# Kernel tuning notes

Measured on AMD Instinct MI355X. Metric: run time of the kernel, lower is better.

The kernel has to match this reference:

```python
import jax, jax.numpy as jnp
import numpy as np

N_HEAD = 16

def setup_inputs() -> dict:
    key = jax.random.key(0)
    ks = jax.random.split(key, 4)
    C = 2048
    x = jax.random.normal(ks[0], (4, 2048, C), dtype=jnp.float32)
    # weights stored [in, out] (transpose of torch Linear's [out, in]); same math y = x @ W + b
    w_qkv = jax.random.normal(ks[1], (C, 3 * C), dtype=jnp.float32) * (1.0 / np.sqrt(C))
    b_qkv = jnp.zeros((3 * C,), dtype=jnp.float32)
    w_proj = jax.random.normal(ks[2], (C, C), dtype=jnp.float32) * (1.0 / np.sqrt(C))
    b_proj = jnp.zeros((C,), dtype=jnp.float32)
    return {"x": x, "w_qkv": w_qkv, "b_qkv": b_qkv, "w_proj": w_proj, "b_proj": b_proj}

def reference(x, w_qkv, b_qkv, w_proj, b_proj):
    B, S, C = x.shape
    H = N_HEAD
    D = C // H
    qkv = x @ w_qkv + b_qkv                      # [B,S,3C]
    q, k, v = jnp.split(qkv, 3, axis=-1)
    # [B,H,S,D]
    q = q.reshape(B, S, H, D).transpose(0, 2, 1, 3)
    k = k.reshape(B, S, H, D).transpose(0, 2, 1, 3)
    v = v.reshape(B, S, H, D).transpose(0, 2, 1, 3)
    scale = 1.0 / np.sqrt(D).astype(np.float32)
    scores = jnp.einsum('bhqd,bhkd->bhqk', q, k) * scale   # [B,H,S,S]
    causal = jnp.tril(jnp.ones((S, S), dtype=bool))
    scores = jnp.where(causal, scores, jnp.finfo(scores.dtype).min)
    attn = jax.nn.softmax(scores, axis=-1)
    y = jnp.einsum('bhqk,bhkd->bhqd', attn, v)              # [B,H,S,D]
    y = y.transpose(0, 2, 1, 3).reshape(B, S, C)
    return y @ w_proj + b_proj
```

## Files before the change

### kernel.cpp

```cpp
#include <hip/hip_runtime.h>
#include <hip/hip_bf16.h>

typedef __bf16 bf16x8 __attribute__((ext_vector_type(8)));
typedef float floatx4 __attribute__((ext_vector_type(4)));

__device__ __forceinline__ unsigned short f2bf(float f) {
  unsigned u = __float_as_uint(f);
  u += 0x7fffu + ((u >> 16) & 1u);
  return (unsigned short)(u >> 16);
}

__device__ __forceinline__ unsigned cvt_pk_bf16(float lo, float hi) {
  unsigned r;
  asm("v_cvt_pk_bf16_f32 %0, %1, %2" : "=v"(r) : "v"(lo), "v"(hi));
  return r;
}

__device__ __forceinline__ void async_copy16(const void* g, void* l) {
  __builtin_amdgcn_global_load_lds(
      (const __attribute__((address_space(1))) void*)g,
      (__attribute__((address_space(3))) void*)l, 16, 0, 0);
}

__global__ __launch_bounds__(256) void cvt_bf16(
    const float* __restrict__ in, unsigned short* __restrict__ out) {
  size_t i = ((size_t)blockIdx.x * 256 + threadIdx.x) * 8;
  float4 a0 = *(const float4*)&in[i];
  float4 a1 = *(const float4*)&in[i + 4];
  uint4 d;
  d.x = (unsigned)f2bf(a0.x) | ((unsigned)f2bf(a0.y) << 16);
  d.y = (unsigned)f2bf(a0.z) | ((unsigned)f2bf(a0.w) << 16);
  d.z = (unsigned)f2bf(a1.x) | ((unsigned)f2bf(a1.y) << 16);
  d.w = (unsigned)f2bf(a1.z) | ((unsigned)f2bf(a1.w) << 16);
  *(uint4*)(&out[i]) = d;
}

__global__ __launch_bounds__(256) void transpose_cvt(
    const float* __restrict__ in, unsigned short* __restrict__ out,
    int R, int Ccol) {
  __shared__ unsigned short tile[32][33];
  int c0 = blockIdx.x * 32, r0 = blockIdx.y * 32;
  int tx = threadIdx.x & 31, ty = threadIdx.x >> 5;
  #pragma unroll
  for (int i = 0; i < 32; i += 8)
    tile[ty + i][tx] = f2bf(in[(size_t)(r0 + ty + i) * Ccol + c0 + tx]);
  __syncthreads();
  #pragma unroll
  for (int i = 0; i < 32; i += 8)
    out[(size_t)(c0 + ty + i) * R + r0 + tx] = tile[tx][ty + i];
}

__device__ __forceinline__ void stage_tile256(
    const unsigned short* __restrict__ A, const unsigned short* __restrict__ Bt,
    int K, int m0, int n0, int k0,
    unsigned short* As, unsigned short* Bs, int lane, int w) {
  const int lrow = lane >> 3;
  const int gch = (lane & 7) ^ lrow;
  #pragma unroll
  for (int u = 0; u < 4; u++) {
    int g = w * 4 + u;
    int row = g * 8 + lrow;
    async_copy16(&A[(size_t)(m0 + row) * K + k0 + gch * 8], &As[g * 512]);
  }
  #pragma unroll
  for (int u = 0; u < 4; u++) {
    int g = w * 4 + u;
    int row = g * 8 + lrow;
    async_copy16(&Bt[(size_t)(n0 + row) * K + k0 + gch * 8], &Bs[g * 512]);
  }
}

__device__ __forceinline__ void gemm_bt_256(
    const unsigned short* __restrict__ A, const unsigned short* __restrict__ Bt,
    int K, int m0, int n0,
    unsigned short* AsB, unsigned short* BsB,
    floatx4 acc[8][4]) {
  const int t = threadIdx.x, lane = t & 63, w = t >> 6;
  const int wr = w >> 2, wc = w & 3;
  const int l15 = lane & 15, l4 = lane >> 4;
  const floatx4 zf = {0.f, 0.f, 0.f, 0.f};
  #pragma unroll
  for (int mi = 0; mi < 8; mi++)
    #pragma unroll
    for (int ni = 0; ni < 4; ni++) acc[mi][ni] = zf;

  const int nkt = K >> 6;
  stage_tile256(A, Bt, K, m0, n0, 0, AsB, BsB, lane, w);
  __syncthreads();

  #pragma unroll 1
  for (int kt = 0; kt < nkt; kt++) {
    const unsigned short* Ab = AsB + (kt & 1) * 16384;
    const unsigned short* Bb = BsB + (kt & 1) * 16384;
    if (kt + 1 < nkt)
      stage_tile256(A, Bt, K, m0, n0, (kt + 1) * 64,
                    AsB + ((kt + 1) & 1) * 16384,
                    BsB + ((kt + 1) & 1) * 16384, lane, w);
    #pragma unroll
    for (int j = 0; j < 4; j++) {
      const int qm = j >> 1, qn = j & 1;
      bf16x8 af[4][2], bfr[2][2];
      #pragma unroll
      for (int mi = 0; mi < 4; mi++) {
        int row = wr * 128 + (qm * 4 + mi) * 16 + l15;
        #pragma unroll
        for (int kk = 0; kk < 2; kk++)
          af[mi][kk] = *(const bf16x8*)(
              &Ab[row * 64 + (((kk * 4 + l4) ^ (l15 & 7)) << 3)]);
      }
      #pragma unroll
      for (int ni = 0; ni < 2; ni++) {
        int row = wc * 64 + (qn * 2 + ni) * 16 + l15;
        #pragma unroll
        for (int kk = 0; kk < 2; kk++)
          bfr[ni][kk] = *(const bf16x8*)(
              &Bb[row * 64 + (((kk * 4 + l4) ^ (l15 & 7)) << 3)]);
      }
      __builtin_amdgcn_s_barrier();
      __builtin_amdgcn_s_setprio(1);
      #pragma unroll
      for (int kk = 0; kk < 2; kk++)
        #pragma unroll
        for (int mi = 0; mi < 4; mi++)
          #pragma unroll
          for (int ni = 0; ni < 2; ni++)
            acc[qm * 4 + mi][qn * 2 + ni] = __builtin_amdgcn_mfma_f32_16x16x32_bf16(
                af[mi][kk], bfr[ni][kk], acc[qm * 4 + mi][qn * 2 + ni], 0, 0, 0);
      __builtin_amdgcn_s_setprio(0);
      if (j < 3) __builtin_amdgcn_s_barrier();
    }
    __syncthreads();
  }
}

__global__ __launch_bounds__(512, 2) void gemm_qkv(
    const unsigned short* __restrict__ X, const unsigned short* __restrict__ WT,
    const float* __restrict__ bias,
    unsigned short* __restrict__ Qo, unsigned short* __restrict__ Ko,
    unsigned short* __restrict__ Vto) {
  __shared__ unsigned short As[2][256 * 64];
  __shared__ unsigned short Bs[2][256 * 64];
  int id = blockIdx.x;
  int n8 = gridDim.x >> 3;
  int lg = (id & 7) * n8 + (id >> 3);
  int bm = lg & 31, bn = lg >> 5;
  int m0 = bm * 256, n0 = bn * 256;
  floatx4 acc[8][4];
  gemm_bt_256(X, WT, 2048, m0, n0, As[0], Bs[0], acc);

  const int t = threadIdx.x, lane = t & 63, w = t >> 6;
  const int wr = w >> 2, wc = w & 3;
  const int l15 = lane & 15, l4 = lane >> 4;
  int which = n0 >> 11;
  int b = m0 >> 11;
  int s0 = m0 & 2047;
  float bv[4];
  #pragma unroll
  for (int ni = 0; ni < 4; ni++)
    bv[ni] = bias[n0 + wc * 64 + ni * 16 + l15];

  if (which < 2) {
    unsigned short* dst = (which == 0) ? Qo : Ko;
    #pragma unroll
    for (int ni = 0; ni < 4; ni++) {
      int cn = (n0 & 2047) + wc * 64 + ni * 16;
      int h = cn >> 7, d = (cn & 127) + l15;
      size_t base = ((size_t)(b * 16 + h)) * 2048;
      #pragma unroll
      for (int mi = 0; mi < 8; mi++) {
        #pragma unroll
        for (int r = 0; r < 4; r++) {
          int srow = s0 + wr * 128 + mi * 16 + l4 * 4 + r;
          dst[(base + srow) * 128 + d] = f2bf(acc[mi][ni][r] + bv[ni]);
        }
      }
    }
  } else {
    #pragma unroll
    for (int ni = 0; ni < 4; ni++) {
      int cn = (n0 & 2047) + wc * 64 + ni * 16;
      int h = cn >> 7, d = (cn & 127) + l15;
      #pragma unroll
      for (int mi = 0; mi < 8; mi++) {
        int sr = s0 + wr * 128 + mi * 16 + l4 * 4;
        ushort4 v;
        v.x = f2bf(acc[mi][ni][0] + bv[ni]);
        v.y = f2bf(acc[mi][ni][1] + bv[ni]);
        v.z = f2bf(acc[mi][ni][2] + bv[ni]);
        v.w = f2bf(acc[mi][ni][3] + bv[ni]);
        *(ushort4*)(&Vto[((size_t)(b * 16 + h) * 128 + d) * 2048 + sr]) = v;
      }
    }
  }
}

__device__ __forceinline__ void attn_stage(
    const unsigned short* __restrict__ Kb, const unsigned short* __restrict__ Vb,
    __bf16* Ksel, __bf16* Vsel, int k0, int lane, int w) {
  const int krow_in = lane >> 4, kch = lane & 15;
  const int vrow_in = lane >> 3, vch = lane & 7;
  #pragma unroll
  for (int u = 0; u < 2; u++) {
    int uk = w * 2 + u;
    int row = uk * 4 + krow_in;
    int sch = kch ^ (row & 7);
    async_copy16(&Kb[(size_t)(k0 + row) * 128 + sch * 8], Ksel + uk * 512);
  }
  #pragma unroll
  for (int u = 0; u < 2; u++) {
    int uv = w * 2 + u;
    int row = uv * 8 + vrow_in;
    int sch = vch ^ vrow_in;
    async_copy16(&Vb[(size_t)row * 2048 + k0 + sch * 8], Vsel + uv * 512);
  }
}

__global__ __launch_bounds__(512, 4) void attn(
    const unsigned short* __restrict__ Qg, const unsigned short* __restrict__ Kg,
    const unsigned short* __restrict__ Vtg, unsigned short* __restrict__ Yg) {
  const int S = 2048, Dh = 128;
  const float c1 = 0.08838834764831845f * 1.4426950408889634f;
  const float NEG_BIG = -3.0e38f;
  __shared__ __bf16 Ks[2][64 * 128];
  __shared__ __bf16 Vs[2][128 * 64];
  __shared__ __bf16 Ps[8][16 * 64];

  int wg = blockIdx.x;
  int lg = (wg & 7) * 64 + (wg >> 3);
  int qtp = lg & 7;
  int bh = lg >> 3;
  const int t = threadIdx.x, lane = t & 63, w = t >> 6;
  const int l15 = lane & 15, l4 = lane >> 4;
  const unsigned short* Qb = Qg + (size_t)bh * S * Dh;
  const unsigned short* Kb = Kg + (size_t)bh * S * Dh;
  const unsigned short* Vb = Vtg + (size_t)bh * Dh * S;
  __bf16* Pw = Ps[w];
  int b = bh >> 4, h = bh & 15;
  const floatx4 zf = {0.f, 0.f, 0.f, 0.f};

  #pragma unroll 1
  for (int half = 0; half < 2; half++) {
    int jq = half ? qtp : (15 - qtp);
    int qb0 = jq * 128;
    int qrow_base = qb0 + w * 16;
    bf16x8 qf[4];
    #pragma unroll
    for (int kk = 0; kk < 4; kk++)
      qf[kk] = *(const bf16x8*)(
          &Qb[(size_t)(qrow_base + l15) * Dh + kk * 32 + l4 * 8]);
    floatx4 accO[8];
    #pragma unroll
    for (int nd = 0; nd < 8; nd++) accO[nd] = zf;
    float mst = NEG_BIG, lst = 0.f;

    int ntiles = 2 * jq + 2;
    int cur = 0;
    attn_stage(Kb, Vb, Ks[0], Vs[0], 0, lane, w);
    __syncthreads();

    #pragma unroll 1
    for (int kt = 0; kt < ntiles; kt++) {
      if (kt + 1 < ntiles)
        attn_stage(Kb, Vb, Ks[cur ^ 1], Vs[cur ^ 1], (kt + 1) * 64, lane, w);

      const __bf16* Kcur = Ks[cur];
      const __bf16* Vcur = Vs[cur];
      floatx4 sc[4];
      #pragma unroll
      for (int ni = 0; ni < 4; ni++) sc[ni] = zf;
      __builtin_amdgcn_s_setprio(1);
      #pragma unroll
      for (int kk = 0; kk < 4; kk++) {
        bf16x8 kf[4];
        #pragma unroll
        for (int ni = 0; ni < 4; ni++) {
          int row = ni * 16 + l15;
          kf[ni] = *(const bf16x8*)(
              &Kcur[row * 128 + (((kk * 4 + l4) ^ (l15 & 7)) << 3)]);
        }
        #pragma unroll
        for (int ni = 0; ni < 4; ni++)
          sc[ni] = __builtin_amdgcn_mfma_f32_16x16x32_bf16(kf[ni], qf[kk], sc[ni], 0, 0, 0);
      }
      __builtin_amdgcn_s_setprio(0);

      if (kt >= 2 * jq) {
        int kb = kt * 64 - qb0 - w * 16 - l15;
        #pragma unroll
        for (int ni = 0; ni < 4; ni++)
          #pragma unroll
          for (int r = 0; r < 4; r++)
            if (kb + ni * 16 + l4 * 4 + r > 0) sc[ni][r] = NEG_BIG;
      }

      float mt = fmaxf(fmaxf(fmaxf(sc[0][0], sc[0][1]), fmaxf(sc[0][2], sc[0][3])),
                       fmaxf(fmaxf(sc[1][0], sc[1][1]), fmaxf(sc[1][2], sc[1][3])));
      mt = fmaxf(mt,
           fmaxf(fmaxf(fmaxf(sc[2][0], sc[2][1]), fmaxf(sc[2][2], sc[2][3])),
                 fmaxf(fmaxf(sc[3][0], sc[3][1]), fmaxf(sc[3][2], sc[3][3]))));
      mt = fmaxf(mt, __shfl_xor(mt, 16, 64));
      mt = fmaxf(mt, __shfl_xor(mt, 32, 64));

      if (!__all(mt <= mst + 8.0f)) {
        float mnew = fmaxf(mst, mt);
        float alpha = exp2f((mst - mnew) * c1);
        mst = mnew;
        lst *= alpha;
        float ar[4];
        #pragma unroll
        for (int r = 0; r < 4; r++)
          ar[r] = __shfl(alpha, l4 * 20 + r, 64);
        #pragma unroll
        for (int nd = 0; nd < 8; nd++)
          #pragma unroll
          for (int r = 0; r < 4; r++) accO[nd][r] *= ar[r];
      }

      float mc = mst * c1;
      float p[4][4];
      float rs = 0.f;
      #pragma unroll
      for (int ni = 0; ni < 4; ni++)
        #pragma unroll
        for (int r = 0; r < 4; r++) {
          p[ni][r] = exp2f(sc[ni][r] * c1 - mc);
          rs += p[ni][r];
        }
      rs += __shfl_xor(rs, 16, 64);
      rs += __shfl_xor(rs, 32, 64);
      lst += rs;

      #pragma unroll
      for (int ni = 0; ni < 4; ni++) {
        uint2 dw;
        dw.x = cvt_pk_bf16(p[ni][0], p[ni][1]);
        dw.y = cvt_pk_bf16(p[ni][2], p[ni][3]);
        int s = ni * 4 + l4;
        *(uint2*)(&Pw[l15 * 64 + (((s >> 1) ^ (l15 & 7)) << 3) + ((s & 1) << 2)]) = dw;
      }

      __builtin_amdgcn_s_setprio(1);
      #pragma unroll
      for (int kk = 0; kk < 2; kk++) {
        bf16x8 pf = *(const bf16x8*)(
            &Pw[l15 * 64 + (((kk * 4 + l4) ^ (l15 & 7)) << 3)]);
        #pragma unroll
        for (int nd = 0; nd < 8; nd++) {
          int row = nd * 16 + l15;
          bf16x8 vf = *(const bf16x8*)(
              &Vcur[row * 64 + (((kk * 4 + l4) ^ (l15 & 7)) << 3)]);
          accO[nd] = __builtin_amdgcn_mfma_f32_16x16x32_bf16(pf, vf, accO[nd], 0, 0, 0);
        }
      }
      __builtin_amdgcn_s_setprio(0);
      __syncthreads();
      cur ^= 1;
    }

    float invl = 1.0f / lst;
    float ivr[4];
    #pragma unroll
    for (int r = 0; r < 4; r++)
      ivr[r] = __shfl(invl, l4 * 20 + r, 64);
    #pragma unroll
    for (int r = 0; r < 4; r++) {
      int srow = qrow_base + l4 * 4 + r;
      size_t rowbase = ((size_t)(b * 2048 + srow)) * 2048 + h * 128;
      #pragma unroll
      for (int nd = 0; nd < 8; nd++)
        Yg[rowbase + nd * 16 + l15] = f2bf(accO[nd][r] * ivr[r]);
    }
  }
}

__global__ __launch_bounds__(512, 2) void gemm_proj(
    const unsigned short* __restrict__ Yin, const unsigned short* __restrict__ WT,
    const float* __restrict__ bias, float* __restrict__ Og) {
  __shared__ unsigned short As[2][256 * 64];
  __shared__ unsigned short Bs[2][256 * 64];
  int id = blockIdx.x;
  int n8 = gridDim.x >> 3;
  int lg = (id & 7) * n8 + (id >> 3);
  int bm = lg & 31, bn = lg >> 5;
  int m0 = bm * 256, n0 = bn * 256;
  floatx4 acc[8][4];
  gemm_bt_256(Yin, WT, 2048, m0, n0, As[0], Bs[0], acc);

  const int t = threadIdx.x, lane = t & 63, w = t >> 6;
  const int wr = w >> 2, wc = w & 3;
  const int l15 = lane & 15, l4 = lane >> 4;
  float bv[4];
  #pragma unroll
  for (int ni = 0; ni < 4; ni++)
    bv[ni] = bias[n0 + wc * 64 + ni * 16 + l15];
  #pragma unroll
  for (int mi = 0; mi < 8; mi++)
    #pragma unroll
    for (int ni = 0; ni < 4; ni++)
      #pragma unroll
      for (int r = 0; r < 4; r++)
        Og[(size_t)(m0 + wr * 128 + mi * 16 + l4 * 4 + r) * 2048 +
           n0 + wc * 64 + ni * 16 + l15] = acc[mi][ni][r] + bv[ni];
}

extern "C" void kernel_launch(void* const* d_in, const int* in_sizes, int n_in,
                              void* d_out, int out_size, void* d_ws, size_t ws_size,
                              hipStream_t stream) {
  const float* x      = (const float*)d_in[0];
  const float* w_qkv  = (const float*)d_in[1];
  const float* b_qkv  = (const float*)d_in[2];
  const float* w_proj = (const float*)d_in[3];
  const float* b_proj = (const float*)d_in[4];
  float* out = (float*)d_out;
  char* ws = (char*)d_ws;

  unsigned short* Q   = (unsigned short*)d_out;
  unsigned short* Kt  = (unsigned short*)((char*)d_out + 33554432);
  unsigned short* Vt  = (unsigned short*)(ws);
  unsigned short* Xbf = (unsigned short*)(ws + 33554432);
  unsigned short* Y   = (unsigned short*)(ws + 33554432);
  unsigned short* WqT = (unsigned short*)(ws + 67108864);
  unsigned short* WpT = (unsigned short*)(ws + 67108864);

  cvt_bf16<<<dim3(8192), 256, 0, stream>>>(x, Xbf);
  transpose_cvt<<<dim3(192, 64), 256, 0, stream>>>(w_qkv, WqT, 2048, 6144);
  gemm_qkv<<<dim3(768), 512, 0, stream>>>(Xbf, WqT, b_qkv, Q, Kt, Vt);
  attn<<<dim3(512), 512, 0, stream>>>(Q, Kt, Vt, Y);
  transpose_cvt<<<dim3(64, 64), 256, 0, stream>>>(w_proj, WpT, 2048, 2048);
  gemm_proj<<<dim3(256), 512, 0, stream>>>(Y, WpT, b_proj, out);
}
```

Measured before the change: 681.6 us.

## Interleave next-tile async loads across MFMA sub-phases and change block-to-tile mapping

The GEMM mainloop now issues the prefetch of the next K-tile in four chunks, one per compute sub-phase, instead of all at once at the start of the iteration. It uses explicit vmcnt waits plus s_barrier in place of the per-iteration __syncthreads, so the wait only covers the current tile's loads. Both GEMMs also drop the XCD-aware block swizzle for a plain row-major grid mapping (bn fastest), which changes L2 locality across chiplets. The finer-grained pipeline spreads memory traffic between MFMA bursts, but the vmcnt accounting and barrier placement must stay exactly right to avoid LDS races.

Measured after the change: 590.0 us. 1.16x faster.

```diff
diff --git a/kernel.cpp b/kernel.cpp
--- a/kernel.cpp
+++ b/kernel.cpp
@@ -50,23 +50,26 @@
     out[(size_t)(c0 + ty + i) * R + r0 + tx] = tile[tx][ty + i];
 }
 
-__device__ __forceinline__ void stage_tile256(
+__device__ __forceinline__ void stage_chunk256(
     const unsigned short* __restrict__ A, const unsigned short* __restrict__ Bt,
     int K, int m0, int n0, int k0,
-    unsigned short* As, unsigned short* Bs, int lane, int w) {
+    unsigned short* As, unsigned short* Bs, int lane, int w, int j) {
   const int lrow = lane >> 3;
   const int gch = (lane & 7) ^ lrow;
-  #pragma unroll
-  for (int u = 0; u < 4; u++) {
-    int g = w * 4 + u;
-    int row = g * 8 + lrow;
-    async_copy16(&A[(size_t)(m0 + row) * K + k0 + gch * 8], &As[g * 512]);
-  }
-  #pragma unroll
-  for (int u = 0; u < 4; u++) {
-    int g = w * 4 + u;
-    int row = g * 8 + lrow;
-    async_copy16(&Bt[(size_t)(n0 + row) * K + k0 + gch * 8], &Bs[g * 512]);
+  if (j < 2) {
+    #pragma unroll
+    for (int u = 2 * j; u < 2 * j + 2; u++) {
+      int g = w * 4 + u;
+      int row = g * 8 + lrow;
+      async_copy16(&A[(size_t)(m0 + row) * K + k0 + gch * 8], &As[g * 512]);
+    }
+  } else {
+    #pragma unroll
+    for (int u = 2 * (j - 2); u < 2 * (j - 2) + 2; u++) {
+      int g = w * 4 + u;
+      int row = g * 8 + lrow;
+      async_copy16(&Bt[(size_t)(n0 + row) * K + k0 + gch * 8], &Bs[g * 512]);
+    }
   }
 }
 
@@ -85,17 +88,24 @@
     for (int ni = 0; ni < 4; ni++) acc[mi][ni] = zf;
 
   const int nkt = K >> 6;
-  stage_tile256(A, Bt, K, m0, n0, 0, AsB, BsB, lane, w);
-  __syncthreads();
+  #pragma unroll
+  for (int j = 0; j < 4; j++)
+    stage_chunk256(A, Bt, K, m0, n0, 0, AsB, BsB, lane, w, j);
 
   #pragma unroll 1
   for (int kt = 0; kt < nkt; kt++) {
     const unsigned short* Ab = AsB + (kt & 1) * 16384;
     const unsigned short* Bb = BsB + (kt & 1) * 16384;
-    if (kt + 1 < nkt)
-      stage_tile256(A, Bt, K, m0, n0, (kt + 1) * 64,
-                    AsB + ((kt + 1) & 1) * 16384,
-                    BsB + ((kt + 1) & 1) * 16384, lane, w);
+    unsigned short* An = AsB + ((kt + 1) & 1) * 16384;
+    unsigned short* Bn = BsB + ((kt + 1) & 1) * 16384;
+    const bool pf = (kt + 1 < nkt);
+    if (pf) {
+      stage_chunk256(A, Bt, K, m0, n0, (kt + 1) * 64, An, Bn, lane, w, 0);
+      asm volatile("s_waitcnt vmcnt(2)" ::: "memory");
+    } else {
+      asm volatile("s_waitcnt vmcnt(0)" ::: "memory");
+    }
+    __builtin_amdgcn_s_barrier();
     #pragma unroll
     for (int j = 0; j < 4; j++) {
       const int qm = j >> 1, qn = j & 1;
@@ -116,6 +126,8 @@
           bfr[ni][kk] = *(const bf16x8*)(
               &Bb[row * 64 + (((kk * 4 + l4) ^ (l15 & 7)) << 3)]);
       }
+      if (j < 3 && pf)
+        stage_chunk256(A, Bt, K, m0, n0, (kt + 1) * 64, An, Bn, lane, w, j + 1);
       __builtin_amdgcn_s_barrier();
       __builtin_amdgcn_s_setprio(1);
       #pragma unroll
@@ -129,8 +141,8 @@
       __builtin_amdgcn_s_setprio(0);
       if (j < 3) __builtin_amdgcn_s_barrier();
     }
-    __syncthreads();
-  }
+  }
+  __builtin_amdgcn_s_barrier();
 }
 
 __global__ __launch_bounds__(512, 2) void gemm_qkv(
@@ -140,10 +152,8 @@
     unsigned short* __restrict__ Vto) {
   __shared__ unsigned short As[2][256 * 64];
   __shared__ unsigned short Bs[2][256 * 64];
-  int id = blockIdx.x;
-  int n8 = gridDim.x >> 3;
-  int lg = (id & 7) * n8 + (id >> 3);
-  int bm = lg & 31, bn = lg >> 5;
+  int lg = blockIdx.x;
+  int bn = lg % 24, bm = lg / 24;
   int m0 = bm * 256, n0 = bn * 256;
   floatx4 acc[8][4];
   gemm_bt_256(X, WT, 2048, m0, n0, As[0], Bs[0], acc);
@@ -378,10 +388,8 @@
     const float* __restrict__ bias, float* __restrict__ Og) {
   __shared__ unsigned short As[2][256 * 64];
   __shared__ unsigned short Bs[2][256 * 64];
-  int id = blockIdx.x;
-  int n8 = gridDim.x >> 3;
-  int lg = (id & 7) * n8 + (id >> 3);
-  int bm = lg & 31, bn = lg >> 5;
+  int lg = blockIdx.x;
+  int bn = lg % 8, bm = lg / 8;
   int m0 = bm * 256, n0 = bn * 256;
   floatx4 acc[8][4];
   gemm_bt_256(Yin, WT, 2048, m0, n0, As[0], Bs[0], acc);
```
